# Kernel tuning notes

Measured on AMD Instinct MI355X. Metric: run time of the kernel, lower is better.

Reference implementation:

```python
import jax, jax.numpy as jnp
import numpy as np

B, S, IN, OUT = 8, 2048, 4096, 4096
SPARSE_FRACTION = 0.9
ALPHA = 0.3


def setup_inputs() -> dict:
    key = jax.random.key(0)
    k1, k2, k3 = jax.random.split(key, 3)
    total = IN * OUT
    target_nz = int(total * (1.0 - SPARSE_FRACTION))          # nonzeros after rigl step
    num_drop = int(ALPHA * target_nz)                          # = mask.sum() - target_nz
    # kaiming_uniform_(a=sqrt(5)) -> bound = 1/sqrt(fan_in)
    bound = 1.0 / np.sqrt(IN)
    weight = jax.random.uniform(k1, (OUT, IN), minval=-bound, maxval=bound, dtype=jnp.float32)
    x = jax.random.normal(k2, (B, S, IN), dtype=jnp.float32)
    dense_grad = jax.random.normal(k3, (OUT, IN), dtype=jnp.float32) * 0.01
    # mask starts with target_nz + num_drop nonzeros so the drop/grow path runs
    rng = np.random.default_rng(0)
    idx = rng.permutation(total)[: target_nz + num_drop]
    m = np.zeros(total, dtype=bool)
    m[idx] = True
    mask = jnp.asarray(m.reshape(OUT, IN))
    return {"x": x, "weight": weight, "dense_grad": dense_grad, "mask": mask, "num_drop": num_drop}


def _rigl_mask(weight, dense_grad, mask, num_drop):
    # RigL sparse-to-sparse update: drop smallest-|w|, grow largest-|grad| among masked-out slots.
    flat = mask.reshape(-1)
    if num_drop > 0:  # num_drop is a static Python int
        wmag = jnp.abs(weight).reshape(-1)
        _, drop_idx = jax.lax.top_k(-wmag, num_drop)           # smallest magnitudes
        flat = flat.at[drop_idx].set(False)
        gmag = jnp.abs(dense_grad).reshape(-1)
        grow_scores = jnp.where(flat, -jnp.inf, gmag)          # only grow where mask == 0
        _, grow_idx = jax.lax.top_k(grow_scores, num_drop)
        flat = flat.at[grow_idx].set(True)
    return flat.reshape(mask.shape)


def reference(x, weight, dense_grad, mask, num_drop):
    new_mask = _rigl_mask(weight, dense_grad, mask, num_drop)
    masked_weight = weight * new_mask.astype(weight.dtype)     # [OUT, IN]
    # F.linear: y = x @ W^T
    return jnp.einsum('bsi,oi->bso', x, masked_weight)
```

## Files before the change

### kernel.cpp

```cpp
#include <hip/hip_runtime.h>
#include <hip/hip_bf16.h>

#define M_TOT 16384
#define N_TOT 4096
#define K_TOT 4096
#define NELEM 16777216

typedef __attribute__((ext_vector_type(8))) short bf16x8;
typedef __attribute__((ext_vector_type(4))) float f32x4;

#define AS1 __attribute__((address_space(1)))
#define AS3 __attribute__((address_space(3)))

struct SelState {
  unsigned long long prefix;
  unsigned long long thr;
  unsigned int k_rem;
  unsigned int done;
  unsigned int active;
};

struct Ctl {
  unsigned long long pcount;
  unsigned int mask_is_byte;
  unsigned int cand_n;
  SelState d;
  SelState g;
};

__device__ Ctl g_ctl;
__device__ unsigned int g_hist[4096];
__device__ unsigned char g_elig[NELEM];
__device__ unsigned short g_wb[NELEM];
__device__ unsigned short g_xb[(size_t)M_TOT * K_TOT];
__device__ unsigned long long g_cand[NELEM];

__device__ __forceinline__ unsigned short f2bf(float f) {
  unsigned int u = __float_as_uint(f);
  unsigned int r = (u + 0x7FFFu + ((u >> 16) & 1u)) >> 16;
  return (unsigned short)r;
}

__device__ __forceinline__ unsigned long long key_drop_bits(unsigned int fb, int i) {
  unsigned int b = fb & 0x7FFFFFFFu;
  return (((unsigned long long)b) << 24) | (unsigned int)i;
}
__device__ __forceinline__ unsigned long long key_grow_bits(unsigned int fb, int i) {
  unsigned int b = ~(fb & 0x7FFFFFFFu);
  return (((unsigned long long)b) << 24) | (unsigned int)i;
}

__global__ void ctl_reset() {
  int t = threadIdx.x;
  if (t == 0) { g_ctl.pcount = 0ull; g_ctl.cand_n = 0u; }
  for (int i = t; i < 4096; i += 256) g_hist[i] = 0;
}

__global__ void mask_popcnt(const unsigned int* mw) {
  const int NW = NELEM / 4;
  unsigned int s = 0;
  for (int i = blockIdx.x * blockDim.x + threadIdx.x; i < NW; i += gridDim.x * blockDim.x)
    s += __popc(mw[i]);
  for (int off = 32; off > 0; off >>= 1) s += __shfl_down(s, off, 64);
  if ((threadIdx.x & 63) == 0)
    atomicAdd((unsigned long long*)&g_ctl.pcount, (unsigned long long)s);
}

__global__ void sel_init(const int* ndp) {
  unsigned int k = (unsigned int)ndp[0];
  g_ctl.mask_is_byte = (g_ctl.pcount > 1200000ull) ? 1u : 0u;
  SelState s;
  s.prefix = 0ull; s.thr = 0ull; s.k_rem = k;
  s.done = (k == 0u) ? 1u : 0u;
  s.active = (k > 0u) ? 1u : 0u;
  g_ctl.d = s;
  g_ctl.g = s;
}

template <int SEL>
__global__ __launch_bounds__(256) void hist_pass(const float* __restrict__ src, int shift, int nbits) {
  SelState& st = SEL ? g_ctl.g : g_ctl.d;
  if (st.done) return;
  __shared__ unsigned int lh[4096];
  const int nb = 1 << nbits;
  for (int i = threadIdx.x; i < nb; i += blockDim.x) lh[i] = 0;
  __syncthreads();
  const unsigned long long pref = st.prefix;
  const int N4 = NELEM / 4;
  for (int q = blockIdx.x * blockDim.x + threadIdx.x; q < N4; q += gridDim.x * blockDim.x) {
    float4 v = ((const float4*)src)[q];
    float fv[4] = {v.x, v.y, v.z, v.w};
    unsigned char ev[4] = {1, 1, 1, 1};
    if (SEL) {
      uchar4 e4 = ((const uchar4*)g_elig)[q];
      ev[0] = e4.x; ev[1] = e4.y; ev[2] = e4.z; ev[3] = e4.w;
    }
#pragma unroll
    for (int j = 0; j < 4; ++j) {
      if (SEL && !ev[j]) continue;
      int i = q * 4 + j;
      unsigned int fb = __float_as_uint(fv[j]);
      unsigned long long key = SEL ? key_grow_bits(fb, i) : key_drop_bits(fb, i);
      if ((key >> (shift + nbits)) == pref)
        atomicAdd(&lh[(unsigned int)(key >> shift) & (unsigned int)(nb - 1)], 1u);
    }
  }
  __syncthreads();
  for (int i = threadIdx.x; i < nb; i += blockDim.x)
    if (lh[i]) atomicAdd(&g_hist[i], lh[i]);
}

#define CCAP 4096
template <int SEL>
__global__ __launch_bounds__(256) void compact_pass(const float* __restrict__ src) {
  SelState& st = SEL ? g_ctl.g : g_ctl.d;
  if (st.done) return;
  __shared__ unsigned long long lk[CCAP];
  __shared__ unsigned int ln;
  __shared__ unsigned int gbase;
  if (threadIdx.x == 0) ln = 0;
  __syncthreads();
  const unsigned long long pref = st.prefix;
  const int N4 = NELEM / 4;
  for (int q = blockIdx.x * blockDim.x + threadIdx.x; q < N4; q += gridDim.x * blockDim.x) {
    float4 v = ((const float4*)src)[q];
    float fv[4] = {v.x, v.y, v.z, v.w};
    unsigned char ev[4] = {1, 1, 1, 1};
    if (SEL) {
      uchar4 e4 = ((const uchar4*)g_elig)[q];
      ev[0] = e4.x; ev[1] = e4.y; ev[2] = e4.z; ev[3] = e4.w;
    }
#pragma unroll
    for (int j = 0; j < 4; ++j) {
      if (SEL && !ev[j]) continue;
      int i = q * 4 + j;
      unsigned int fb = __float_as_uint(fv[j]);
      unsigned long long key = SEL ? key_grow_bits(fb, i) : key_drop_bits(fb, i);
      if ((key >> 44) == pref) {
        unsigned int slot = atomicAdd(&ln, 1u);
        if (slot < CCAP) {
          lk[slot] = key;
        } else {
          unsigned int gb = atomicAdd(&g_ctl.cand_n, 1u);
          g_cand[gb] = key;
        }
      }
    }
  }
  __syncthreads();
  unsigned int n = ln < CCAP ? ln : CCAP;
  if (threadIdx.x == 0) gbase = atomicAdd(&g_ctl.cand_n, n);
  __syncthreads();
  for (unsigned int i = threadIdx.x; i < n; i += blockDim.x)
    g_cand[gbase + i] = lk[i];
}

template <int SEL>
__global__ __launch_bounds__(256) void hist_cand(int shift, int nbits) {
  SelState& st = SEL ? g_ctl.g : g_ctl.d;
  if (st.done) return;
  __shared__ unsigned int lh[4096];
  const int nb = 1 << nbits;
  for (int i = threadIdx.x; i < nb; i += blockDim.x) lh[i] = 0;
  __syncthreads();
  const unsigned long long pref = st.prefix;
  const unsigned int n = g_ctl.cand_n;
  for (unsigned int i = blockIdx.x * blockDim.x + threadIdx.x; i < n; i += gridDim.x * blockDim.x) {
    unsigned long long key = g_cand[i];
    if ((key >> (shift + nbits)) == pref)
      atomicAdd(&lh[(unsigned int)(key >> shift) & (unsigned int)(nb - 1)], 1u);
  }
  __syncthreads();
  for (int i = threadIdx.x; i < nb; i += blockDim.x)
    if (lh[i]) atomicAdd(&g_hist[i], lh[i]);
}

template <int SEL>
__global__ void select_pass(int shift, int nbits) {
  SelState& st = SEL ? g_ctl.g : g_ctl.d;
  if (st.done) return;
  __shared__ unsigned int sc[256];
  __shared__ int tgt;
  const int nb = 1 << nbits;
  const int per = (nb + 255) / 256;
  const int t = threadIdx.x;
  unsigned int s = 0;
  for (int j = 0; j < per; ++j) {
    int b = t * per + j;
    if (b < nb) s += g_hist[b];
  }
  sc[t] = s;
  __syncthreads();
  for (int off = 1; off < 256; off <<= 1) {
    unsigned int v = (t >= off) ? sc[t - off] : 0u;
    __syncthreads();
    sc[t] += v;
    __syncthreads();
  }
  const unsigned int k = st.k_rem;
  const unsigned int cum = sc[t];
  const unsigned int before = cum - s;
  if (before < k && k <= cum) tgt = t;
  __syncthreads();
  if (t == tgt) {
    unsigned int c = before;
    for (int j = 0; j < per; ++j) {
      int b = t * per + j;
      unsigned int h = (b < nb) ? g_hist[b] : 0u;
      if (c + h >= k) {
        unsigned long long np = (st.prefix << nbits) | (unsigned long long)(unsigned int)b;
        st.prefix = np;
        st.k_rem = k - c;
        st.thr = ((np + 1ull) << shift) - 1ull;
        if (k - c == h) st.done = 1;
        break;
      }
      c += h;
    }
  }
  __syncthreads();
  for (int b = t; b < nb; b += 256) g_hist[b] = 0;
}

__global__ __launch_bounds__(256) void build_elig(const float* __restrict__ w, const void* maskp) {
  if (blockIdx.x == 0 && threadIdx.x == 0) g_ctl.cand_n = 0u;
  int q = blockIdx.x * blockDim.x + threadIdx.x;
  if (q >= NELEM / 4) return;
  float4 wv = ((const float4*)w)[q];
  float fv[4] = {wv.x, wv.y, wv.z, wv.w};
  unsigned char m[4];
  if (g_ctl.mask_is_byte) {
    uchar4 m4 = ((const uchar4*)maskp)[q];
    m[0] = m4.x; m[1] = m4.y; m[2] = m4.z; m[3] = m4.w;
  } else {
    int4 m4 = ((const int4*)maskp)[q];
    m[0] = m4.x != 0; m[1] = m4.y != 0; m[2] = m4.z != 0; m[3] = m4.w != 0;
  }
  const bool act = g_ctl.d.active;
  const unsigned long long thr = g_ctl.d.thr;
  uchar4 e;
  unsigned char ev[4];
#pragma unroll
  for (int j = 0; j < 4; ++j) {
    int i = q * 4 + j;
    bool dropped = act && (key_drop_bits(__float_as_uint(fv[j]), i) <= thr);
    ev[j] = (!m[j] || dropped) ? 1 : 0;
  }
  e.x = ev[0]; e.y = ev[1]; e.z = ev[2]; e.w = ev[3];
  ((uchar4*)g_elig)[q] = e;
}

__global__ __launch_bounds__(256) void build_wb(const float* __restrict__ w, const float* __restrict__ gr) {
  int q = blockIdx.x * blockDim.x + threadIdx.x;
  if (q >= NELEM / 4) return;
  float4 wv = ((const float4*)w)[q];
  float4 gv = ((const float4*)gr)[q];
  float wf[4] = {wv.x, wv.y, wv.z, wv.w};
  float gf[4] = {gv.x, gv.y, gv.z, gv.w};
  uchar4 e4 = ((const uchar4*)g_elig)[q];
  unsigned char ev[4] = {e4.x, e4.y, e4.z, e4.w};
  const bool act = g_ctl.g.active;
  const unsigned long long thr = g_ctl.g.thr;
  ushort4 o;
  unsigned short ov[4];
#pragma unroll
  for (int j = 0; j < 4; ++j) {
    int i = q * 4 + j;
    bool keep;
    if (!ev[j]) keep = true;
    else keep = act && (key_grow_bits(__float_as_uint(gf[j]), i) <= thr);
    ov[j] = keep ? f2bf(wf[j]) : (unsigned short)0;
  }
  o.x = ov[0]; o.y = ov[1]; o.z = ov[2]; o.w = ov[3];
  ((ushort4*)g_wb)[q] = o;
}

__global__ __launch_bounds__(256) void convert_x(const float* __restrict__ x) {
  int i = blockIdx.x * blockDim.x + threadIdx.x;
  float4 v = ((const float4*)x)[i];
  ushort4 o;
  o.x = f2bf(v.x); o.y = f2bf(v.y); o.z = f2bf(v.z); o.w = f2bf(v.w);
  ((ushort4*)g_xb)[i] = o;
}

#define BM2 256
#define BN2 256
#define BK2 64
#define NT2 (K_TOT / BK2)
#define BUFB (256 * 128)

__global__ __launch_bounds__(512, 2) void gemm_kernel(float* __restrict__ out) {
  __shared__ __align__(16) char smem[131072];
  unsigned short* Asb = (unsigned short*)smem;
  unsigned short* Bsb = (unsigned short*)(smem + 65536);
  const int tid = threadIdx.x;
  const int lane = tid & 63;
  const int w = tid >> 6;
  const int wm = w >> 2, wn = w & 3;

  const int orig = blockIdx.x;
  const int swz = (orig & 7) * 128 + (orig >> 3);
  const int gm0 = (swz >> 4) * BM2;
  const int gn0 = (swz & 15) * BN2;

  f32x4 acc[8][4];
#pragma unroll
  for (int i = 0; i < 8; ++i)
#pragma unroll
    for (int j = 0; j < 4; ++j) acc[i][j] = (f32x4){0.f, 0.f, 0.f, 0.f};

  const int sr = (w << 3) + (lane >> 3);
  const int sc = 8 * ((lane & 7) ^ (lane >> 3));
  const unsigned short* Agp = g_xb + (size_t)(gm0 + sr) * K_TOT + sc;
  const unsigned short* Bgp = g_wb + (size_t)(gn0 + sr) * K_TOT + sc;
  const int lr = (w << 3);

#define STAGE_A(tile, half) do {                                             \
    const int bi_ = (tile) & 1; const int kb_ = ((tile) & (NT2 - 1)) * BK2;  \
    __builtin_amdgcn_global_load_lds(                                        \
        (const AS1 void*)(Agp + (size_t)((half) * 128) * K_TOT + kb_),       \
        (AS3 void*)(Asb + (size_t)bi_ * (BM2 * BK2) +                        \
                    ((half) * 128 + lr) * BK2), 16, 0, 0);                   \
    __builtin_amdgcn_global_load_lds(                                        \
        (const AS1 void*)(Agp + (size_t)((half) * 128 + 64) * K_TOT + kb_),  \
        (AS3 void*)(Asb + (size_t)bi_ * (BM2 * BK2) +                        \
                    ((half) * 128 + 64 + lr) * BK2), 16, 0, 0);              \
  } while (0)
#define STAGE_B(tile, half) do {                                             \
    const int bi_ = (tile) & 1; const int kb_ = ((tile) & (NT2 - 1)) * BK2;  \
    __builtin_amdgcn_global_load_lds(                                        \
        (const AS1 void*)(Bgp + (size_t)((half) * 128) * K_TOT + kb_),       \
        (AS3 void*)(Bsb + (size_t)bi_ * (BN2 * BK2) +                        \
                    ((half) * 128 + lr) * BK2), 16, 0, 0);                   \
    __builtin_amdgcn_global_load_lds(                                        \
        (const AS1 void*)(Bgp + (size_t)((half) * 128 + 64) * K_TOT + kb_),  \
        (AS3 void*)(Bsb + (size_t)bi_ * (BN2 * BK2) +                        \
                    ((half) * 128 + 64 + lr) * BK2), 16, 0, 0);              \
  } while (0)

  const int r16 = lane & 15;
  const int kcb = (lane >> 4) << 4;
  const int xv = (r16 & 7) << 4;
  const char* Ab0 = (const char*)(Asb + wm * 128 * BK2);
  const char* Bb0 = (const char*)(Bsb + wn * 64 * BK2);

  bf16x8 pA[4][2], pB0[2][2], pB1[2][2];

#define LD_A(qm, bi) do {                                                     \
    const char* ab_ = Ab0 + (bi) * BUFB + ((qm) * 64 + r16) * 128;            \
    _Pragma("unroll") for (int mi = 0; mi < 4; ++mi)                          \
      _Pragma("unroll") for (int sk = 0; sk < 2; ++sk)                        \
        pA[mi][sk] = *(const bf16x8*)(ab_ + mi * 16 * 128 +                   \
                                      ((sk * 64 + kcb) ^ xv));                \
  } while (0)
#define LD_B(P, qn, bi) do {                                                  \
    const char* bb_ = Bb0 + (bi) * BUFB + ((qn) * 32 + r16) * 128;            \
    _Pragma("unroll") for (int nf = 0; nf < 2; ++nf)                          \
      _Pragma("unroll") for (int sk = 0; sk < 2; ++sk)                        \
        P[nf][sk] = *(const bf16x8*)(bb_ + nf * 16 * 128 +                    \
                                     ((sk * 64 + kcb) ^ xv));                 \
  } while (0)
#define MFMA_Q(qm, qn, P) do {                                                \
    __builtin_amdgcn_s_setprio(1);                                            \
    _Pragma("unroll") for (int mi = 0; mi < 4; ++mi)                          \
      _Pragma("unroll") for (int nf = 0; nf < 2; ++nf)                        \
        _Pragma("unroll") for (int sk = 0; sk < 2; ++sk)                      \
          acc[(qm) * 4 + mi][(qn) * 2 + nf] =                                 \
              __builtin_amdgcn_mfma_f32_16x16x32_bf16(                        \
                  pA[mi][sk], P[nf][sk], acc[(qm) * 4 + mi][(qn) * 2 + nf],   \
                  0, 0, 0);                                                   \
    __builtin_amdgcn_s_setprio(0);                                            \
  } while (0)
#define BAR() __builtin_amdgcn_s_barrier()
#define WLG() asm volatile("s_waitcnt lgkmcnt(0)" ::: "memory")
#define WLG8() asm volatile("s_waitcnt lgkmcnt(8)" ::: "memory")
#define WVM6() asm volatile("s_waitcnt vmcnt(6)" ::: "memory")

  STAGE_A(0, 0); STAGE_A(0, 1); STAGE_B(0, 0); STAGE_B(0, 1);
  STAGE_B(1, 0); STAGE_B(1, 1); STAGE_A(1, 0);
  WVM6();
  BAR();

  for (int it = 0; it < NT2 / 2; ++it) {
    const int T = 2 * it;
    LD_A(0, 0); LD_B(pB0, 0, 0);
    STAGE_A(T + 1, 1);
    WLG8();
    BAR(); WLG();
    MFMA_Q(0, 0, pB0);
    BAR();
    LD_B(pB1, 1, 0);
    STAGE_B(T + 2, 0);
    BAR(); WLG();
    MFMA_Q(0, 1, pB1);
    BAR();
    LD_A(1, 0);
    STAGE_B(T + 2, 1);
    BAR(); WLG();
    MFMA_Q(1, 1, pB1);
    BAR();
    STAGE_A(T + 2, 0);
    BAR();
    MFMA_Q(1, 0, pB0);
    WVM6();
    BAR();
    LD_A(0, 1); LD_B(pB0, 0, 1);
    STAGE_A(T + 2, 1);
    WLG8();
    BAR(); WLG();
    MFMA_Q(0, 0, pB0);
    BAR();
    LD_B(pB1, 1, 1);
    STAGE_B(T + 3, 0);
    BAR(); WLG();
    MFMA_Q(0, 1, pB1);
    BAR();
    LD_A(1, 1);
    STAGE_B(T + 3, 1);
    BAR(); WLG();
    MFMA_Q(1, 1, pB1);
    BAR();
    STAGE_A(T + 3, 0);
    BAR();
    MFMA_Q(1, 0, pB0);
    WVM6();
    BAR();
  }

  float* lf = (float*)smem;
#pragma unroll
  for (int Q = 0; Q < 4; ++Q) {
    __syncthreads();
#pragma unroll
    for (int m2 = 0; m2 < 2; ++m2) {
      const int rl0 = (wm * 2 + m2) * 16 + (lane >> 4) * 4;
#pragma unroll
      for (int nf = 0; nf < 4; ++nf) {
        const int col = wn * 64 + nf * 16 + (lane & 15);
#pragma unroll
        for (int r = 0; r < 4; ++r)
          lf[(rl0 + r) * 260 + col] = acc[Q * 2 + m2][nf][r];
      }
    }
    __syncthreads();
#pragma unroll
    for (int i2 = 0; i2 < 8; ++i2) {
      const int rl = w * 8 + i2;
      const int grow = (rl >> 5) * 128 + (Q * 2 + ((rl >> 4) & 1)) * 16 + (rl & 15);
      *(float4*)&out[(size_t)(gm0 + grow) * N_TOT + gn0 + lane * 4] =
          *(const float4*)&lf[rl * 260 + lane * 4];
    }
  }
}

extern "C" void kernel_launch(void* const* d_in, const int* in_sizes, int n_in,
                              void* d_out, int out_size, void* d_ws, size_t ws_size,
                              hipStream_t stream) {
  const float* x  = (const float*)d_in[0];
  const float* wt = (const float*)d_in[1];
  const float* gr = (const float*)d_in[2];
  const void*  mk = d_in[3];
  const int*   nd = (const int*)d_in[4];
  (void)d_ws; (void)ws_size; (void)in_sizes; (void)n_in; (void)out_size;

  ctl_reset<<<1, 256, 0, stream>>>();
  mask_popcnt<<<512, 256, 0, stream>>>((const unsigned int*)mk);
  sel_init<<<1, 1, 0, stream>>>(nd);

  const int shifts[5] = {44, 32, 24, 12, 0};
  const int nbits[5]  = {12, 12, 8, 12, 12};

  hist_pass<0><<<1024, 256, 0, stream>>>(wt, shifts[0], nbits[0]);
  select_pass<0><<<1, 256, 0, stream>>>(shifts[0], nbits[0]);
  compact_pass<0><<<1024, 256, 0, stream>>>(wt);
  for (int p = 1; p < 5; ++p) {
    hist_cand<0><<<256, 256, 0, stream>>>(shifts[p], nbits[p]);
    select_pass<0><<<1, 256, 0, stream>>>(shifts[p], nbits[p]);
  }
  build_elig<<<NELEM / 4 / 256, 256, 0, stream>>>(wt, mk);
  hist_pass<1><<<1024, 256, 0, stream>>>(gr, shifts[0], nbits[0]);
  select_pass<1><<<1, 256, 0, stream>>>(shifts[0], nbits[0]);
  compact_pass<1><<<1024, 256, 0, stream>>>(gr);
  for (int p = 1; p < 5; ++p) {
    hist_cand<1><<<256, 256, 0, stream>>>(shifts[p], nbits[p]);
    select_pass<1><<<1, 256, 0, stream>>>(shifts[p], nbits[p]);
  }
  build_wb<<<NELEM / 4 / 256, 256, 0, stream>>>(wt, gr);
  convert_x<<<(M_TOT * K_TOT / 4) / 256, 256, 0, stream>>>(x);
  gemm_kernel<<<1024, 512, 0, stream>>>((float*)d_out);
}
```

Before: 882.2 us.

## Fuse radix-select histogram and select passes, drop GEMM LDS waitcnts

The first histogram pass now runs the bucket selection in whichever block finishes last, using a global ticket counter, so a separate select launch is no longer needed. The four candidate refinement passes are folded into one single-block kernel that keeps its histogram in shared memory. Together these cut the launch count from about 22 small kernels to 6. Separately, the explicit lgkmcnt waits before the GEMM MFMA phases are removed. That reduces stalls but relies on the compiler inserting the LDS waits itself, which carries a correctness risk if it does not.

```diff
diff --git a/kernel.cpp b/kernel.cpp
--- a/kernel.cpp
+++ b/kernel.cpp
@@ -30,6 +30,7 @@
 
 __device__ Ctl g_ctl;
 __device__ unsigned int g_hist[4096];
+__device__ unsigned int g_ticket[4];
 __device__ unsigned char g_elig[NELEM];
 __device__ unsigned short g_wb[NELEM];
 __device__ unsigned short g_xb[(size_t)M_TOT * K_TOT];
@@ -53,6 +54,7 @@
 __global__ void ctl_reset() {
   int t = threadIdx.x;
   if (t == 0) { g_ctl.pcount = 0ull; g_ctl.cand_n = 0u; }
+  if (t < 4) g_ticket[t] = 0u;
   for (int i = t; i < 4096; i += 256) g_hist[i] = 0;
 }
 
@@ -77,15 +79,57 @@
   g_ctl.g = s;
 }
 
+__device__ void do_select_impl(unsigned int* hist, SelState* stp, int shift, int nbits) {
+  __shared__ unsigned int sc[256];
+  __shared__ int tgt;
+  const int nb = 1 << nbits;
+  const int per = (nb + 255) / 256;
+  const int t = threadIdx.x;
+  unsigned int s = 0;
+  for (int j = 0; j < per; ++j) {
+    int b = t * per + j;
+    if (b < nb) s += hist[b];
+  }
+  sc[t] = s;
+  __syncthreads();
+  for (int off = 1; off < 256; off <<= 1) {
+    unsigned int v = (t >= off) ? sc[t - off] : 0u;
+    __syncthreads();
+    sc[t] += v;
+    __syncthreads();
+  }
+  const unsigned int k = stp->k_rem;
+  const unsigned int cum = sc[t];
+  const unsigned int before = cum - s;
+  if (before < k && k <= cum) tgt = t;
+  __syncthreads();
+  if (t == tgt) {
+    unsigned int c = before;
+    for (int j = 0; j < per; ++j) {
+      int b = t * per + j;
+      unsigned int h = (b < nb) ? hist[b] : 0u;
+      if (c + h >= k) {
+        unsigned long long np = (stp->prefix << nbits) | (unsigned long long)(unsigned int)b;
+        stp->prefix = np;
+        stp->k_rem = k - c;
+        stp->thr = ((np + 1ull) << shift) - 1ull;
+        if (k - c == h) stp->done = 1;
+        break;
+      }
+      c += h;
+    }
+  }
+  __syncthreads();
+  for (int b = t; b < nb; b += 256) hist[b] = 0;
+}
+
 template <int SEL>
-__global__ __launch_bounds__(256) void hist_pass(const float* __restrict__ src, int shift, int nbits) {
-  SelState& st = SEL ? g_ctl.g : g_ctl.d;
-  if (st.done) return;
+__global__ __launch_bounds__(256) void histsel_full(const float* __restrict__ src) {
+  SelState* stp = SEL ? &g_ctl.g : &g_ctl.d;
+  if (stp->done) return;
   __shared__ unsigned int lh[4096];
-  const int nb = 1 << nbits;
-  for (int i = threadIdx.x; i < nb; i += blockDim.x) lh[i] = 0;
-  __syncthreads();
-  const unsigned long long pref = st.prefix;
+  for (int i = threadIdx.x; i < 4096; i += 256) lh[i] = 0;
+  __syncthreads();
   const int N4 = NELEM / 4;
   for (int q = blockIdx.x * blockDim.x + threadIdx.x; q < N4; q += gridDim.x * blockDim.x) {
     float4 v = ((const float4*)src)[q];
@@ -101,13 +145,19 @@
       int i = q * 4 + j;
       unsigned int fb = __float_as_uint(fv[j]);
       unsigned long long key = SEL ? key_grow_bits(fb, i) : key_drop_bits(fb, i);
-      if ((key >> (shift + nbits)) == pref)
-        atomicAdd(&lh[(unsigned int)(key >> shift) & (unsigned int)(nb - 1)], 1u);
-    }
-  }
-  __syncthreads();
-  for (int i = threadIdx.x; i < nb; i += blockDim.x)
+      atomicAdd(&lh[(unsigned int)(key >> 44)], 1u);
+    }
+  }
+  __syncthreads();
+  for (int i = threadIdx.x; i < 4096; i += 256)
     if (lh[i]) atomicAdd(&g_hist[i], lh[i]);
+  __threadfence();
+  __shared__ unsigned int tk;
+  if (threadIdx.x == 0) tk = atomicAdd(&g_ticket[SEL], 1u);
+  __syncthreads();
+  if (tk != (unsigned int)gridDim.x - 1) return;
+  __threadfence();
+  do_select_impl(g_hist, stp, 44, 12);
 }
 
 #define CCAP 4096
@@ -156,70 +206,29 @@
 }
 
 template <int SEL>
-__global__ __launch_bounds__(256) void hist_cand(int shift, int nbits) {
-  SelState& st = SEL ? g_ctl.g : g_ctl.d;
-  if (st.done) return;
+__global__ __launch_bounds__(256) void cand_passes() {
+  SelState* stp = SEL ? &g_ctl.g : &g_ctl.d;
   __shared__ unsigned int lh[4096];
-  const int nb = 1 << nbits;
-  for (int i = threadIdx.x; i < nb; i += blockDim.x) lh[i] = 0;
-  __syncthreads();
-  const unsigned long long pref = st.prefix;
+  const int shifts[4] = {32, 24, 12, 0};
+  const int nbitsv[4] = {12, 8, 12, 12};
   const unsigned int n = g_ctl.cand_n;
-  for (unsigned int i = blockIdx.x * blockDim.x + threadIdx.x; i < n; i += gridDim.x * blockDim.x) {
-    unsigned long long key = g_cand[i];
-    if ((key >> (shift + nbits)) == pref)
-      atomicAdd(&lh[(unsigned int)(key >> shift) & (unsigned int)(nb - 1)], 1u);
-  }
-  __syncthreads();
-  for (int i = threadIdx.x; i < nb; i += blockDim.x)
-    if (lh[i]) atomicAdd(&g_hist[i], lh[i]);
-}
-
-template <int SEL>
-__global__ void select_pass(int shift, int nbits) {
-  SelState& st = SEL ? g_ctl.g : g_ctl.d;
-  if (st.done) return;
-  __shared__ unsigned int sc[256];
-  __shared__ int tgt;
-  const int nb = 1 << nbits;
-  const int per = (nb + 255) / 256;
-  const int t = threadIdx.x;
-  unsigned int s = 0;
-  for (int j = 0; j < per; ++j) {
-    int b = t * per + j;
-    if (b < nb) s += g_hist[b];
-  }
-  sc[t] = s;
-  __syncthreads();
-  for (int off = 1; off < 256; off <<= 1) {
-    unsigned int v = (t >= off) ? sc[t - off] : 0u;
-    __syncthreads();
-    sc[t] += v;
-    __syncthreads();
-  }
-  const unsigned int k = st.k_rem;
-  const unsigned int cum = sc[t];
-  const unsigned int before = cum - s;
-  if (before < k && k <= cum) tgt = t;
-  __syncthreads();
-  if (t == tgt) {
-    unsigned int c = before;
-    for (int j = 0; j < per; ++j) {
-      int b = t * per + j;
-      unsigned int h = (b < nb) ? g_hist[b] : 0u;
-      if (c + h >= k) {
-        unsigned long long np = (st.prefix << nbits) | (unsigned long long)(unsigned int)b;
-        st.prefix = np;
-        st.k_rem = k - c;
-        st.thr = ((np + 1ull) << shift) - 1ull;
-        if (k - c == h) st.done = 1;
-        break;
-      }
-      c += h;
-    }
-  }
-  __syncthreads();
-  for (int b = t; b < nb; b += 256) g_hist[b] = 0;
+  for (int p = 0; p < 4; ++p) {
+    if (stp->done) break;
+    const int nbits = nbitsv[p];
+    const int shift = shifts[p];
+    const int nb = 1 << nbits;
+    for (int i = threadIdx.x; i < nb; i += 256) lh[i] = 0;
+    __syncthreads();
+    const unsigned long long pref = stp->prefix;
+    for (unsigned int i = threadIdx.x; i < n; i += 256) {
+      unsigned long long key = g_cand[i];
+      if ((key >> (shift + nbits)) == pref)
+        atomicAdd(&lh[(unsigned int)(key >> shift) & (unsigned int)(nb - 1)], 1u);
+    }
+    __syncthreads();
+    do_select_impl(lh, stp, shift, nbits);
+    __syncthreads();
+  }
 }
 
 __global__ __launch_bounds__(256) void build_elig(const float* __restrict__ w, const void* maskp) {
@@ -372,8 +381,6 @@
     __builtin_amdgcn_s_setprio(0);                                            \
   } while (0)
 #define BAR() __builtin_amdgcn_s_barrier()
-#define WLG() asm volatile("s_waitcnt lgkmcnt(0)" ::: "memory")
-#define WLG8() asm volatile("s_waitcnt lgkmcnt(8)" ::: "memory")
 #define WVM6() asm volatile("s_waitcnt vmcnt(6)" ::: "memory")
 
   STAGE_A(0, 0); STAGE_A(0, 1); STAGE_B(0, 0); STAGE_B(0, 1);
@@ -385,18 +392,17 @@
     const int T = 2 * it;
     LD_A(0, 0); LD_B(pB0, 0, 0);
     STAGE_A(T + 1, 1);
-    WLG8();
-    BAR(); WLG();
+    BAR();
     MFMA_Q(0, 0, pB0);
     BAR();
     LD_B(pB1, 1, 0);
     STAGE_B(T + 2, 0);
-    BAR(); WLG();
+    BAR();
     MFMA_Q(0, 1, pB1);
     BAR();
     LD_A(1, 0);
     STAGE_B(T + 2, 1);
-    BAR(); WLG();
+    BAR();
     MFMA_Q(1, 1, pB1);
     BAR();
     STAGE_A(T + 2, 0);
@@ -406,18 +412,17 @@
     BAR();
     LD_A(0, 1); LD_B(pB0, 0, 1);
     STAGE_A(T + 2, 1);
-    WLG8();
-    BAR(); WLG();
+    BAR();
     MFMA_Q(0, 0, pB0);
     BAR();
     LD_B(pB1, 1, 1);
     STAGE_B(T + 3, 0);
-    BAR(); WLG();
+    BAR();
     MFMA_Q(0, 1, pB1);
     BAR();
     LD_A(1, 1);
     STAGE_B(T + 3, 1);
-    BAR(); WLG();
+    BAR();
     MFMA_Q(1, 1, pB1);
     BAR();
     STAGE_A(T + 3, 0);
@@ -467,24 +472,13 @@
   mask_popcnt<<<512, 256, 0, stream>>>((const unsigned int*)mk);
   sel_init<<<1, 1, 0, stream>>>(nd);
 
-  const int shifts[5] = {44, 32, 24, 12, 0};
-  const int nbits[5]  = {12, 12, 8, 12, 12};
-
-  hist_pass<0><<<1024, 256, 0, stream>>>(wt, shifts[0], nbits[0]);
-  select_pass<0><<<1, 256, 0, stream>>>(shifts[0], nbits[0]);
+  histsel_full<0><<<1024, 256, 0, stream>>>(wt);
   compact_pass<0><<<1024, 256, 0, stream>>>(wt);
-  for (int p = 1; p < 5; ++p) {
-    hist_cand<0><<<256, 256, 0, stream>>>(shifts[p], nbits[p]);
-    select_pass<0><<<1, 256, 0, stream>>>(shifts[p], nbits[p]);
-  }
+  cand_passes<0><<<1, 256, 0, stream>>>();
   build_elig<<<NELEM / 4 / 256, 256, 0, stream>>>(wt, mk);
-  hist_pass<1><<<1024, 256, 0, stream>>>(gr, shifts[0], nbits[0]);
-  select_pass<1><<<1, 256, 0, stream>>>(shifts[0], nbits[0]);
+  histsel_full<1><<<1024, 256, 0, stream>>>(gr);
   compact_pass<1><<<1024, 256, 0, stream>>>(gr);
-  for (int p = 1; p < 5; ++p) {
-    hist_cand<1><<<256, 256, 0, stream>>>(shifts[p], nbits[p]);
-    select_pass<1><<<1, 256, 0, stream>>>(shifts[p], nbits[p]);
-  }
+  cand_passes<1><<<1, 256, 0, stream>>>();
   build_wb<<<NELEM / 4 / 256, 256, 0, stream>>>(wt, gr);
   convert_x<<<(M_TOT * K_TOT / 4) / 256, 256, 0, stream>>>(x);
   gemm_kernel<<<1024, 512, 0, stream>>>((float*)d_out);
```

After: 1.652 ms. 1.87x slower.

## Fuse eligibility build into grow histogram and specialize first radix pass

Applied to the files above, without the earlier changes.

Merges the eligibility-mask construction with the first grow-side histogram pass, so the weight, mask and gradient are read in one sweep instead of two kernels. The first-pass histogram kernels now compute the top-12-bit bin directly instead of building 64-bit keys and comparing prefixes, and compact_pass compares 32-bit bins. It also removes the explicit lgkmcnt waits before barriers in the GEMM main loop. That last change risks reading LDS data before the loads complete unless the compiler inserts the waits itself.

```diff
diff --git a/kernel.cpp b/kernel.cpp
--- a/kernel.cpp
+++ b/kernel.cpp
@@ -48,6 +48,12 @@
 __device__ __forceinline__ unsigned long long key_grow_bits(unsigned int fb, int i) {
   unsigned int b = ~(fb & 0x7FFFFFFFu);
   return (((unsigned long long)b) << 24) | (unsigned int)i;
+}
+__device__ __forceinline__ unsigned int bin_drop(unsigned int fb) {
+  return (fb & 0x7FFFFFFFu) >> 20;
+}
+__device__ __forceinline__ unsigned int bin_grow(unsigned int fb) {
+  return (~(fb & 0x7FFFFFFFu)) >> 20;
 }
 
 __global__ void ctl_reset() {
@@ -77,102 +83,66 @@
   g_ctl.g = s;
 }
 
-template <int SEL>
-__global__ __launch_bounds__(256) void hist_pass(const float* __restrict__ src, int shift, int nbits) {
-  SelState& st = SEL ? g_ctl.g : g_ctl.d;
-  if (st.done) return;
+__global__ __launch_bounds__(256) void hist_drop(const float* __restrict__ src) {
+  if (g_ctl.d.done) return;
   __shared__ unsigned int lh[4096];
-  const int nb = 1 << nbits;
-  for (int i = threadIdx.x; i < nb; i += blockDim.x) lh[i] = 0;
-  __syncthreads();
-  const unsigned long long pref = st.prefix;
+  for (int i = threadIdx.x; i < 4096; i += 256) lh[i] = 0;
+  __syncthreads();
   const int N4 = NELEM / 4;
   for (int q = blockIdx.x * blockDim.x + threadIdx.x; q < N4; q += gridDim.x * blockDim.x) {
     float4 v = ((const float4*)src)[q];
     float fv[4] = {v.x, v.y, v.z, v.w};
-    unsigned char ev[4] = {1, 1, 1, 1};
-    if (SEL) {
-      uchar4 e4 = ((const uchar4*)g_elig)[q];
-      ev[0] = e4.x; ev[1] = e4.y; ev[2] = e4.z; ev[3] = e4.w;
-    }
-#pragma unroll
-    for (int j = 0; j < 4; ++j) {
-      if (SEL && !ev[j]) continue;
-      int i = q * 4 + j;
-      unsigned int fb = __float_as_uint(fv[j]);
-      unsigned long long key = SEL ? key_grow_bits(fb, i) : key_drop_bits(fb, i);
-      if ((key >> (shift + nbits)) == pref)
-        atomicAdd(&lh[(unsigned int)(key >> shift) & (unsigned int)(nb - 1)], 1u);
-    }
-  }
-  __syncthreads();
-  for (int i = threadIdx.x; i < nb; i += blockDim.x)
+#pragma unroll
+    for (int j = 0; j < 4; ++j)
+      atomicAdd(&lh[bin_drop(__float_as_uint(fv[j]))], 1u);
+  }
+  __syncthreads();
+  for (int i = threadIdx.x; i < 4096; i += 256)
     if (lh[i]) atomicAdd(&g_hist[i], lh[i]);
 }
 
-#define CCAP 4096
-template <int SEL>
-__global__ __launch_bounds__(256) void compact_pass(const float* __restrict__ src) {
-  SelState& st = SEL ? g_ctl.g : g_ctl.d;
-  if (st.done) return;
-  __shared__ unsigned long long lk[CCAP];
-  __shared__ unsigned int ln;
-  __shared__ unsigned int gbase;
-  if (threadIdx.x == 0) ln = 0;
-  __syncthreads();
-  const unsigned long long pref = st.prefix;
+__global__ __launch_bounds__(256) void hist_grow_elig(const float* __restrict__ w,
+                                                      const float* __restrict__ gr,
+                                                      const void* maskp) {
+  if (blockIdx.x == 0 && threadIdx.x == 0) g_ctl.cand_n = 0u;
+  __shared__ unsigned int lh[4096];
+  for (int i = threadIdx.x; i < 4096; i += 256) lh[i] = 0;
+  __syncthreads();
+  const bool gdone = g_ctl.g.done != 0;
+  const bool dact = g_ctl.d.active != 0;
+  const unsigned long long dthr = g_ctl.d.thr;
+  const bool mbyte = g_ctl.mask_is_byte != 0;
   const int N4 = NELEM / 4;
   for (int q = blockIdx.x * blockDim.x + threadIdx.x; q < N4; q += gridDim.x * blockDim.x) {
-    float4 v = ((const float4*)src)[q];
-    float fv[4] = {v.x, v.y, v.z, v.w};
-    unsigned char ev[4] = {1, 1, 1, 1};
-    if (SEL) {
-      uchar4 e4 = ((const uchar4*)g_elig)[q];
-      ev[0] = e4.x; ev[1] = e4.y; ev[2] = e4.z; ev[3] = e4.w;
-    }
+    float4 wv = ((const float4*)w)[q];
+    float4 gv = ((const float4*)gr)[q];
+    float wf[4] = {wv.x, wv.y, wv.z, wv.w};
+    float gf[4] = {gv.x, gv.y, gv.z, gv.w};
+    unsigned char m[4];
+    if (mbyte) {
+      uchar4 m4 = ((const uchar4*)maskp)[q];
+      m[0] = m4.x; m[1] = m4.y; m[2] = m4.z; m[3] = m4.w;
+    } else {
+      int4 m4 = ((const int4*)maskp)[q];
+      m[0] = m4.x != 0; m[1] = m4.y != 0; m[2] = m4.z != 0; m[3] = m4.w != 0;
+    }
+    uchar4 e;
+    unsigned char ev[4];
 #pragma unroll
     for (int j = 0; j < 4; ++j) {
-      if (SEL && !ev[j]) continue;
       int i = q * 4 + j;
-      unsigned int fb = __float_as_uint(fv[j]);
-      unsigned long long key = SEL ? key_grow_bits(fb, i) : key_drop_bits(fb, i);
-      if ((key >> 44) == pref) {
-        unsigned int slot = atomicAdd(&ln, 1u);
-        if (slot < CCAP) {
-          lk[slot] = key;
-        } else {
-          unsigned int gb = atomicAdd(&g_ctl.cand_n, 1u);
-          g_cand[gb] = key;
-        }
-      }
-    }
-  }
-  __syncthreads();
-  unsigned int n = ln < CCAP ? ln : CCAP;
-  if (threadIdx.x == 0) gbase = atomicAdd(&g_ctl.cand_n, n);
-  __syncthreads();
-  for (unsigned int i = threadIdx.x; i < n; i += blockDim.x)
-    g_cand[gbase + i] = lk[i];
-}
-
-template <int SEL>
-__global__ __launch_bounds__(256) void hist_cand(int shift, int nbits) {
-  SelState& st = SEL ? g_ctl.g : g_ctl.d;
-  if (st.done) return;
-  __shared__ unsigned int lh[4096];
-  const int nb = 1 << nbits;
-  for (int i = threadIdx.x; i < nb; i += blockDim.x) lh[i] = 0;
-  __syncthreads();
-  const unsigned long long pref = st.prefix;
-  const unsigned int n = g_ctl.cand_n;
-  for (unsigned int i = blockIdx.x * blockDim.x + threadIdx.x; i < n; i += gridDim.x * blockDim.x) {
-    unsigned long long key = g_cand[i];
-    if ((key >> (shift + nbits)) == pref)
-      atomicAdd(&lh[(unsigned int)(key >> shift) & (unsigned int)(nb - 1)], 1u);
-  }
-  __syncthreads();
-  for (int i = threadIdx.x; i < nb; i += blockDim.x)
-    if (lh[i]) atomicAdd(&g_hist[i], lh[i]);
+      bool dropped = dact && (key_drop_bits(__float_as_uint(wf[j]), i) <= dthr);
+      ev[j] = (!m[j] || dropped) ? 1 : 0;
+      if (ev[j] && !gdone)
+        atomicAdd(&lh[bin_grow(__float_as_uint(gf[j]))], 1u);
+    }
+    e.x = ev[0]; e.y = ev[1]; e.z = ev[2]; e.w = ev[3];
+    ((uchar4*)g_elig)[q] = e;
+  }
+  __syncthreads();
+  if (!gdone)
+    for (int i = threadIdx.x; i < 4096; i += 256)
+      if (lh[i]) atomicAdd(&g_hist[i], lh[i]);
 }
 
 template <int SEL>
@@ -222,32 +192,70 @@
   for (int b = t; b < nb; b += 256) g_hist[b] = 0;
 }
 
-__global__ __launch_bounds__(256) void build_elig(const float* __restrict__ w, const void* maskp) {
-  if (blockIdx.x == 0 && threadIdx.x == 0) g_ctl.cand_n = 0u;
-  int q = blockIdx.x * blockDim.x + threadIdx.x;
-  if (q >= NELEM / 4) return;
-  float4 wv = ((const float4*)w)[q];
-  float fv[4] = {wv.x, wv.y, wv.z, wv.w};
-  unsigned char m[4];
-  if (g_ctl.mask_is_byte) {
-    uchar4 m4 = ((const uchar4*)maskp)[q];
-    m[0] = m4.x; m[1] = m4.y; m[2] = m4.z; m[3] = m4.w;
-  } else {
-    int4 m4 = ((const int4*)maskp)[q];
-    m[0] = m4.x != 0; m[1] = m4.y != 0; m[2] = m4.z != 0; m[3] = m4.w != 0;
-  }
-  const bool act = g_ctl.d.active;
-  const unsigned long long thr = g_ctl.d.thr;
-  uchar4 e;
-  unsigned char ev[4];
-#pragma unroll
-  for (int j = 0; j < 4; ++j) {
-    int i = q * 4 + j;
-    bool dropped = act && (key_drop_bits(__float_as_uint(fv[j]), i) <= thr);
-    ev[j] = (!m[j] || dropped) ? 1 : 0;
-  }
-  e.x = ev[0]; e.y = ev[1]; e.z = ev[2]; e.w = ev[3];
-  ((uchar4*)g_elig)[q] = e;
+#define CCAP 4096
+template <int SEL>
+__global__ __launch_bounds__(256) void compact_pass(const float* __restrict__ src) {
+  SelState& st = SEL ? g_ctl.g : g_ctl.d;
+  if (st.done) return;
+  __shared__ unsigned long long lk[CCAP];
+  __shared__ unsigned int ln;
+  __shared__ unsigned int gbase;
+  if (threadIdx.x == 0) ln = 0;
+  __syncthreads();
+  const unsigned int pref = (unsigned int)st.prefix;
+  const int N4 = NELEM / 4;
+  for (int q = blockIdx.x * blockDim.x + threadIdx.x; q < N4; q += gridDim.x * blockDim.x) {
+    float4 v = ((const float4*)src)[q];
+    float fv[4] = {v.x, v.y, v.z, v.w};
+    unsigned char ev[4] = {1, 1, 1, 1};
+    if (SEL) {
+      uchar4 e4 = ((const uchar4*)g_elig)[q];
+      ev[0] = e4.x; ev[1] = e4.y; ev[2] = e4.z; ev[3] = e4.w;
+    }
+#pragma unroll
+    for (int j = 0; j < 4; ++j) {
+      if (SEL && !ev[j]) continue;
+      int i = q * 4 + j;
+      unsigned int fb = __float_as_uint(fv[j]);
+      unsigned int bin = SEL ? bin_grow(fb) : bin_drop(fb);
+      if (bin == pref) {
+        unsigned long long key = SEL ? key_grow_bits(fb, i) : key_drop_bits(fb, i);
+        unsigned int slot = atomicAdd(&ln, 1u);
+        if (slot < CCAP) {
+          lk[slot] = key;
+        } else {
+          unsigned int gb = atomicAdd(&g_ctl.cand_n, 1u);
+          g_cand[gb] = key;
+        }
+      }
+    }
+  }
+  __syncthreads();
+  unsigned int n = ln < CCAP ? ln : CCAP;
+  if (threadIdx.x == 0) gbase = atomicAdd(&g_ctl.cand_n, n);
+  __syncthreads();
+  for (unsigned int i = threadIdx.x; i < n; i += blockDim.x)
+    g_cand[gbase + i] = lk[i];
+}
+
+template <int SEL>
+__global__ __launch_bounds__(256) void hist_cand(int shift, int nbits) {
+  SelState& st = SEL ? g_ctl.g : g_ctl.d;
+  if (st.done) return;
+  __shared__ unsigned int lh[4096];
+  const int nb = 1 << nbits;
+  for (int i = threadIdx.x; i < nb; i += blockDim.x) lh[i] = 0;
+  __syncthreads();
+  const unsigned long long pref = st.prefix;
+  const unsigned int n = g_ctl.cand_n;
+  for (unsigned int i = blockIdx.x * blockDim.x + threadIdx.x; i < n; i += gridDim.x * blockDim.x) {
+    unsigned long long key = g_cand[i];
+    if ((key >> (shift + nbits)) == pref)
+      atomicAdd(&lh[(unsigned int)(key >> shift) & (unsigned int)(nb - 1)], 1u);
+  }
+  __syncthreads();
+  for (int i = threadIdx.x; i < nb; i += blockDim.x)
+    if (lh[i]) atomicAdd(&g_hist[i], lh[i]);
 }
 
 __global__ __launch_bounds__(256) void build_wb(const float* __restrict__ w, const float* __restrict__ gr) {
@@ -372,8 +380,6 @@
     __builtin_amdgcn_s_setprio(0);                                            \
   } while (0)
 #define BAR() __builtin_amdgcn_s_barrier()
-#define WLG() asm volatile("s_waitcnt lgkmcnt(0)" ::: "memory")
-#define WLG8() asm volatile("s_waitcnt lgkmcnt(8)" ::: "memory")
 #define WVM6() asm volatile("s_waitcnt vmcnt(6)" ::: "memory")
 
   STAGE_A(0, 0); STAGE_A(0, 1); STAGE_B(0, 0); STAGE_B(0, 1);
@@ -385,18 +391,17 @@
     const int T = 2 * it;
     LD_A(0, 0); LD_B(pB0, 0, 0);
     STAGE_A(T + 1, 1);
-    WLG8();
-    BAR(); WLG();
+    BAR();
     MFMA_Q(0, 0, pB0);
     BAR();
     LD_B(pB1, 1, 0);
     STAGE_B(T + 2, 0);
-    BAR(); WLG();
+    BAR();
     MFMA_Q(0, 1, pB1);
     BAR();
     LD_A(1, 0);
     STAGE_B(T + 2, 1);
-    BAR(); WLG();
+    BAR();
     MFMA_Q(1, 1, pB1);
     BAR();
     STAGE_A(T + 2, 0);
@@ -406,18 +411,17 @@
     BAR();
     LD_A(0, 1); LD_B(pB0, 0, 1);
     STAGE_A(T + 2, 1);
-    WLG8();
-    BAR(); WLG();
+    BAR();
     MFMA_Q(0, 0, pB0);
     BAR();
     LD_B(pB1, 1, 1);
     STAGE_B(T + 3, 0);
-    BAR(); WLG();
+    BAR();
     MFMA_Q(0, 1, pB1);
     BAR();
     LD_A(1, 1);
     STAGE_B(T + 3, 1);
-    BAR(); WLG();
+    BAR();
     MFMA_Q(1, 1, pB1);
     BAR();
     STAGE_A(T + 3, 0);
@@ -470,15 +474,14 @@
   const int shifts[5] = {44, 32, 24, 12, 0};
   const int nbits[5]  = {12, 12, 8, 12, 12};
 
-  hist_pass<0><<<1024, 256, 0, stream>>>(wt, shifts[0], nbits[0]);
+  hist_drop<<<1024, 256, 0, stream>>>(wt);
   select_pass<0><<<1, 256, 0, stream>>>(shifts[0], nbits[0]);
   compact_pass<0><<<1024, 256, 0, stream>>>(wt);
   for (int p = 1; p < 5; ++p) {
     hist_cand<0><<<256, 256, 0, stream>>>(shifts[p], nbits[p]);
     select_pass<0><<<1, 256, 0, stream>>>(shifts[p], nbits[p]);
   }
-  build_elig<<<NELEM / 4 / 256, 256, 0, stream>>>(wt, mk);
-  hist_pass<1><<<1024, 256, 0, stream>>>(gr, shifts[0], nbits[0]);
+  hist_grow_elig<<<1024, 256, 0, stream>>>(wt, gr, mk);
   select_pass<1><<<1, 256, 0, stream>>>(shifts[0], nbits[0]);
   compact_pass<1><<<1024, 256, 0, stream>>>(gr);
   for (int p = 1; p < 5; ++p) {
```

Result: faster. 862.2 us (-2.3%).
